# Optimization experiments

Measured on AMD Instinct MI355X. Metric: run time of the kernel, lower is better.

Reference implementation:

```python
import jax, jax.numpy as jnp
from jax import lax
import numpy as np

B, IN, OUT = 32768, 512, 512


def _bit_length(a):
    # a: nonnegative int32. Smear high bit down, then popcount == bit length.
    y = a
    y = y | (y >> 1)
    y = y | (y >> 2)
    y = y | (y >> 4)
    y = y | (y >> 8)
    y = y | (y >> 16)
    return lax.population_count(y)


def trunc_top_bits(v, k=4):
    # compress_top4(|a|,|b|,4): keep top-k significant bits of each magnitude.
    a = jnp.abs(v)
    shift = jnp.maximum(_bit_length(a) - k, 0)
    t = (a >> shift) << shift
    return t * jnp.sign(v)


def setup_inputs() -> dict:
    key = jax.random.key(0)
    k1, k2, k3 = jax.random.split(key, 3)
    bound = 1.0 / np.sqrt(IN)  # matches kaiming_uniform(a=sqrt(5)) + bias bound
    x = jax.random.normal(k1, (B, IN), dtype=jnp.float32)
    weight = jax.random.uniform(k2, (OUT, IN), dtype=jnp.float32, minval=-bound, maxval=bound)
    bias = jax.random.uniform(k3, (OUT,), dtype=jnp.float32, minval=-bound, maxval=bound)
    return {"x": x, "weight": weight, "bias": bias, "weight_sf": 8, "act_sf": 6}


def reference(x, weight, bias, weight_sf, act_sf):
    # Fixed-point quantization: input / 2^{-sf} then trunc-toward-zero int cast
    xi = (x * (2.0 ** act_sf)).astype(jnp.int32)       # [B, IN]
    wi = (weight * (2.0 ** weight_sf)).astype(jnp.int32)  # [OUT, IN]
    # sign/abs decomposition + top-4-bit truncated multiply-accumulate:
    # sum_y compress_top4(|xi|,|wi|) * sign(xi)*sign(wi) == dot of signed truncs
    tx = trunc_top_bits(xi).astype(jnp.float32)
    tw = trunc_top_bits(wi).astype(jnp.float32)
    acc = jnp.einsum("bi,oi->bo", tx, tw)             # [B, OUT], exact in fp32
    scale = (2.0 ** (-act_sf)) * (2.0 ** (-weight_sf))
    return acc * scale + bias[None, :]
```

## Files before the change

kernel.cpp:

```cpp
#include <hip/hip_runtime.h>
#include <hip/hip_bf16.h>
#include <stdint.h>

#define B_DIM 32768
#define IN_DIM 512
#define OUT_DIM 512

typedef __bf16 bf16;
typedef bf16 bf16x8 __attribute__((ext_vector_type(8)));
typedef float f32x4 __attribute__((ext_vector_type(4)));

__device__ __forceinline__ uint32_t quant2(float a, float b, float scale) {
    uint32_t ua = __float_as_uint(truncf(a * scale));
    uint32_t ub = __float_as_uint(truncf(b * scale));
    uint32_t p = __builtin_amdgcn_perm(ub, ua, 0x07060302u);
    return p & 0xFFF0FFF0u;
}

__global__ void quant_kernel(const float* __restrict__ in, bf16* __restrict__ out,
                             int n4, const int* __restrict__ sf) {
    int i = blockIdx.x * blockDim.x + threadIdx.x;
    if (i >= n4) return;
    float scale = (float)(1 << *sf);
    float4 v = ((const float4*)in)[i];
    uint2 p;
    p.x = quant2(v.x, v.y, scale);
    p.y = quant2(v.z, v.w, scale);
    ((uint2*)out)[i] = p;
}

__global__ __launch_bounds__(256, 4)
void gemm_bt(const bf16* __restrict__ A, const bf16* __restrict__ W,
             const float* __restrict__ bias, float* __restrict__ C,
             const int* __restrict__ wsf, const int* __restrict__ asf) {
    __shared__ bf16 As[128 * 64];
    __shared__ bf16 Bs[128 * 64];

    const int t    = threadIdx.x;
    const int w    = t >> 6;
    const int lane = t & 63;

    const int b    = blockIdx.x;
    const int xcd  = b & 7;
    const int slot = b >> 3;
    const int bm   = xcd * 32 + (slot >> 2);
    const int bn   = slot & 3;
    const int row0 = bm * 128;
    const int col0 = bn * 128;
    const int wm   = (w & 1) * 64;
    const int wn   = (w >> 1) * 64;

    const int m_st = t >> 3;
    const int ku   = (t & 7) ^ (m_st & 7);
    const size_t offA = (size_t)(row0 + m_st) * IN_DIM + ku * 8;
    const size_t offB = (size_t)(col0 + m_st) * IN_DIM + ku * 8;

    f32x4 acc[4][4];
    #pragma unroll
    for (int mt = 0; mt < 4; ++mt)
        #pragma unroll
        for (int nt = 0; nt < 4; ++nt)
            acc[mt][nt] = 0.0f;

    for (int k0 = 0; k0 < IN_DIM; k0 += 64) {
        #pragma unroll
        for (int i = 0; i < 4; ++i) {
            const bf16* ga = A + offA + (size_t)i * 32 * IN_DIM + k0;
            bf16*       la = As + (i * 256 + w * 64) * 8;
            __builtin_amdgcn_global_load_lds((const __attribute__((address_space(1))) void*)ga,
                                             (__attribute__((address_space(3))) void*)la, 16, 0, 0);
            const bf16* gb = W + offB + (size_t)i * 32 * IN_DIM + k0;
            bf16*       lb = Bs + (i * 256 + w * 64) * 8;
            __builtin_amdgcn_global_load_lds((const __attribute__((address_space(1))) void*)gb,
                                             (__attribute__((address_space(3))) void*)lb, 16, 0, 0);
        }
        __syncthreads();

        const int q  = lane >> 4;
        const int rl = lane & 15;
        const int sx = rl & 7;
        #pragma unroll
        for (int ks = 0; ks < 2; ++ks) {
            const int c = ks * 4 + q;
            const int cs = (c ^ sx) * 8;
            bf16x8 af[4], bfr[4];
            #pragma unroll
            for (int mt = 0; mt < 4; ++mt)
                af[mt] = *(const bf16x8*)(As + (wm + mt * 16 + rl) * 64 + cs);
            #pragma unroll
            for (int nt = 0; nt < 4; ++nt)
                bfr[nt] = *(const bf16x8*)(Bs + (wn + nt * 16 + rl) * 64 + cs);
            #pragma unroll
            for (int mt = 0; mt < 4; ++mt)
                #pragma unroll
                for (int nt = 0; nt < 4; ++nt)
                    acc[mt][nt] = __builtin_amdgcn_mfma_f32_16x16x32_bf16(af[mt], bfr[nt], acc[mt][nt], 0, 0, 0);
        }
        __syncthreads();
    }

    const float oscale = ldexpf(1.0f, -(*wsf + *asf));
    const int cl = lane & 15;
    const int rg = (lane >> 4) * 4;
    #pragma unroll
    for (int nt = 0; nt < 4; ++nt) {
        const int col = col0 + wn + nt * 16 + cl;
        const float bv = bias[col];
        #pragma unroll
        for (int mt = 0; mt < 4; ++mt) {
            f32x4 a = acc[mt][nt];
            #pragma unroll
            for (int r = 0; r < 4; ++r) {
                const int row = row0 + wm + mt * 16 + rg + r;
                C[(size_t)row * OUT_DIM + col] = a[r] * oscale + bv;
            }
        }
    }
}

extern "C" void kernel_launch(void* const* d_in, const int* in_sizes, int n_in,
                              void* d_out, int out_size, void* d_ws, size_t ws_size,
                              hipStream_t stream) {
    const float* x    = (const float*)d_in[0];
    const float* wgt  = (const float*)d_in[1];
    const float* bias = (const float*)d_in[2];
    const int*   wsf  = (const int*)d_in[3];
    const int*   asf  = (const int*)d_in[4];

    bf16* tx = (bf16*)d_ws;
    bf16* tw = (bf16*)((char*)d_ws + (size_t)B_DIM * IN_DIM * sizeof(bf16));

    const int nx4 = B_DIM * IN_DIM / 4;
    const int nw4 = OUT_DIM * IN_DIM / 4;
    quant_kernel<<<(nx4 + 255) / 256, 256, 0, stream>>>(x, tx, nx4, asf);
    quant_kernel<<<(nw4 + 255) / 256, 256, 0, stream>>>(wgt, tw, nw4, wsf);

    const int grid = (B_DIM / 128) * (OUT_DIM / 128);
    gemm_bt<<<grid, 256, 0, stream>>>(tx, tw, bias, (float*)d_out, wsf, asf);
}
```

Measured before the change: 137.7 us.

## Fuse activation quantization into GEMM with register-prefetched fp32 tiles

Drops the separate quantization pass over the activation matrix. The GEMM now reads fp32 X directly, quantizes it to truncated bf16 in registers and writes the result into the swizzled LDS tile. The next k-tile is prefetched into registers while the current one computes, and the occupancy hint drops from 4 to 3 waves. This removes a full write and re-read of the bf16 intermediate, but each X tile is now read in fp32 by the four column blocks, and the A operand no longer uses asynchronous global-to-LDS loads.

```diff
diff --git a/kernel.cpp b/kernel.cpp
--- a/kernel.cpp
+++ b/kernel.cpp
@@ -29,10 +29,10 @@
     ((uint2*)out)[i] = p;
 }
 
-__global__ __launch_bounds__(256, 4)
-void gemm_bt(const bf16* __restrict__ A, const bf16* __restrict__ W,
-             const float* __restrict__ bias, float* __restrict__ C,
-             const int* __restrict__ wsf, const int* __restrict__ asf) {
+__global__ __launch_bounds__(256, 3)
+void gemm_fused(const float* __restrict__ X, const bf16* __restrict__ W,
+                const float* __restrict__ bias, float* __restrict__ C,
+                const int* __restrict__ wsf, const int* __restrict__ asf) {
     __shared__ bf16 As[128 * 64];
     __shared__ bf16 Bs[128 * 64];
 
@@ -51,9 +51,14 @@
     const int wn   = (w >> 1) * 64;
 
     const int m_st = t >> 3;
-    const int ku   = (t & 7) ^ (m_st & 7);
-    const size_t offA = (size_t)(row0 + m_st) * IN_DIM + ku * 8;
-    const size_t offB = (size_t)(col0 + m_st) * IN_DIM + ku * 8;
+    const int kub  = (t & 7) ^ (m_st & 7);
+    const size_t offB = (size_t)(col0 + m_st) * IN_DIM + kub * 8;
+
+    const int r_a = t >> 1;
+    const int h_a = t & 1;
+    const float* xrow = X + (size_t)(row0 + r_a) * IN_DIM + h_a * 32;
+
+    const float ascale = (float)(1 << *asf);
 
     f32x4 acc[4][4];
     #pragma unroll
@@ -62,26 +67,55 @@
         for (int nt = 0; nt < 4; ++nt)
             acc[mt][nt] = 0.0f;
 
+    float4 fr[8];
+    #pragma unroll
+    for (int j = 0; j < 8; ++j)
+        fr[j] = *((const float4*)xrow + j);
+    uint4 pk[4];
+    #pragma unroll
+    for (int j = 0; j < 4; ++j) {
+        pk[j].x = quant2(fr[2 * j].x, fr[2 * j].y, ascale);
+        pk[j].y = quant2(fr[2 * j].z, fr[2 * j].w, ascale);
+        pk[j].z = quant2(fr[2 * j + 1].x, fr[2 * j + 1].y, ascale);
+        pk[j].w = quant2(fr[2 * j + 1].z, fr[2 * j + 1].w, ascale);
+    }
+
     for (int k0 = 0; k0 < IN_DIM; k0 += 64) {
         #pragma unroll
+        for (int j = 0; j < 4; ++j) {
+            bf16* adst = As + (size_t)(r_a * 8 + ((h_a * 4 + j) ^ (r_a & 7))) * 8;
+            *(uint4*)adst = pk[j];
+        }
+        #pragma unroll
         for (int i = 0; i < 4; ++i) {
-            const bf16* ga = A + offA + (size_t)i * 32 * IN_DIM + k0;
-            bf16*       la = As + (i * 256 + w * 64) * 8;
-            __builtin_amdgcn_global_load_lds((const __attribute__((address_space(1))) void*)ga,
-                                             (__attribute__((address_space(3))) void*)la, 16, 0, 0);
             const bf16* gb = W + offB + (size_t)i * 32 * IN_DIM + k0;
             bf16*       lb = Bs + (i * 256 + w * 64) * 8;
             __builtin_amdgcn_global_load_lds((const __attribute__((address_space(1))) void*)gb,
                                              (__attribute__((address_space(3))) void*)lb, 16, 0, 0);
         }
+        const bool more = (k0 + 64) < IN_DIM;
+        if (more) {
+            #pragma unroll
+            for (int j = 0; j < 8; ++j)
+                fr[j] = *((const float4*)(xrow + k0 + 64) + j);
+        }
         __syncthreads();
+        if (more) {
+            #pragma unroll
+            for (int j = 0; j < 4; ++j) {
+                pk[j].x = quant2(fr[2 * j].x, fr[2 * j].y, ascale);
+                pk[j].y = quant2(fr[2 * j].z, fr[2 * j].w, ascale);
+                pk[j].z = quant2(fr[2 * j + 1].x, fr[2 * j + 1].y, ascale);
+                pk[j].w = quant2(fr[2 * j + 1].z, fr[2 * j + 1].w, ascale);
+            }
+        }
 
         const int q  = lane >> 4;
         const int rl = lane & 15;
         const int sx = rl & 7;
         #pragma unroll
         for (int ks = 0; ks < 2; ++ks) {
-            const int c = ks * 4 + q;
+            const int c  = ks * 4 + q;
             const int cs = (c ^ sx) * 8;
             bf16x8 af[4], bfr[4];
             #pragma unroll
@@ -127,14 +161,11 @@
     const int*   wsf  = (const int*)d_in[3];
     const int*   asf  = (const int*)d_in[4];
 
-    bf16* tx = (bf16*)d_ws;
-    bf16* tw = (bf16*)((char*)d_ws + (size_t)B_DIM * IN_DIM * sizeof(bf16));
+    bf16* tw = (bf16*)d_ws;
 
-    const int nx4 = B_DIM * IN_DIM / 4;
     const int nw4 = OUT_DIM * IN_DIM / 4;
-    quant_kernel<<<(nx4 + 255) / 256, 256, 0, stream>>>(x, tx, nx4, asf);
     quant_kernel<<<(nw4 + 255) / 256, 256, 0, stream>>>(wgt, tw, nw4, wsf);
 
     const int grid = (B_DIM / 128) * (OUT_DIM / 128);
-    gemm_bt<<<grid, 256, 0, stream>>>(tx, tw, bias, (float*)d_out, wsf, asf);
+    gemm_fused<<<grid, 256, 0, stream>>>(x, tw, bias, (float*)d_out, wsf, asf);
 }
```

Result: slower. 155.4 us (+12.8%).

## Quantize operands to FP8 and use FP8 MFMA instead of BF16

Applied to the files above, without the earlier changes.

The quantize kernels now write the top-4-bit truncated values as packed e4m3 FP8 bytes instead of BF16. The GEMM loads byte tiles into LDS with a reworked swizzle and uses the 16x16x32 FP8 MFMA. This halves the bytes written by the quantize pass and read by the GEMM. It relies on every truncated value fitting exactly in e4m3, meaning 3 mantissa bits and a maximum magnitude below 448. It also changes the LDS access pattern, which could introduce bank conflicts.

```diff
diff --git a/kernel.cpp b/kernel.cpp
--- a/kernel.cpp
+++ b/kernel.cpp
@@ -1,40 +1,35 @@
 #include <hip/hip_runtime.h>
-#include <hip/hip_bf16.h>
 #include <stdint.h>
 
 #define B_DIM 32768
 #define IN_DIM 512
 #define OUT_DIM 512
 
-typedef __bf16 bf16;
-typedef bf16 bf16x8 __attribute__((ext_vector_type(8)));
 typedef float f32x4 __attribute__((ext_vector_type(4)));
 
-__device__ __forceinline__ uint32_t quant2(float a, float b, float scale) {
-    uint32_t ua = __float_as_uint(truncf(a * scale));
-    uint32_t ub = __float_as_uint(truncf(b * scale));
-    uint32_t p = __builtin_amdgcn_perm(ub, ua, 0x07060302u);
-    return p & 0xFFF0FFF0u;
+__device__ __forceinline__ float trunc4(float x, float s) {
+    uint32_t u = __float_as_uint(truncf(x * s));
+    return __uint_as_float(u & 0xFFF00000u);
 }
 
-__global__ void quant_kernel(const float* __restrict__ in, bf16* __restrict__ out,
-                             int n4, const int* __restrict__ sf) {
+__global__ void quant_fp8(const float* __restrict__ in, uint32_t* __restrict__ out,
+                          int n4, const int* __restrict__ sf) {
     int i = blockIdx.x * blockDim.x + threadIdx.x;
     if (i >= n4) return;
     float scale = (float)(1 << *sf);
     float4 v = ((const float4*)in)[i];
-    uint2 p;
-    p.x = quant2(v.x, v.y, scale);
-    p.y = quant2(v.z, v.w, scale);
-    ((uint2*)out)[i] = p;
+    int p = 0;
+    p = __builtin_amdgcn_cvt_pk_fp8_f32(trunc4(v.x, scale), trunc4(v.y, scale), p, false);
+    p = __builtin_amdgcn_cvt_pk_fp8_f32(trunc4(v.z, scale), trunc4(v.w, scale), p, true);
+    out[i] = (uint32_t)p;
 }
 
 __global__ __launch_bounds__(256, 4)
-void gemm_bt(const bf16* __restrict__ A, const bf16* __restrict__ W,
+void gemm_f8(const uint8_t* __restrict__ A, const uint8_t* __restrict__ W,
              const float* __restrict__ bias, float* __restrict__ C,
              const int* __restrict__ wsf, const int* __restrict__ asf) {
-    __shared__ bf16 As[128 * 64];
-    __shared__ bf16 Bs[128 * 64];
+    __shared__ uint8_t As[128 * 64];
+    __shared__ uint8_t Bs[128 * 64];
 
     const int t    = threadIdx.x;
     const int w    = t >> 6;
@@ -50,10 +45,10 @@
     const int wm   = (w & 1) * 64;
     const int wn   = (w >> 1) * 64;
 
-    const int m_st = t >> 3;
-    const int ku   = (t & 7) ^ (m_st & 7);
-    const size_t offA = (size_t)(row0 + m_st) * IN_DIM + ku * 8;
-    const size_t offB = (size_t)(col0 + m_st) * IN_DIM + ku * 8;
+    const int m_st = t >> 2;
+    const int goff = ((2 * (t & 3)) ^ (m_st & 6)) * 8;
+    const size_t offA = (size_t)(row0 + m_st) * IN_DIM + goff;
+    const size_t offB = (size_t)(col0 + m_st) * IN_DIM + goff;
 
     f32x4 acc[4][4];
     #pragma unroll
@@ -64,13 +59,13 @@
 
     for (int k0 = 0; k0 < IN_DIM; k0 += 64) {
         #pragma unroll
-        for (int i = 0; i < 4; ++i) {
-            const bf16* ga = A + offA + (size_t)i * 32 * IN_DIM + k0;
-            bf16*       la = As + (i * 256 + w * 64) * 8;
+        for (int i = 0; i < 2; ++i) {
+            const uint8_t* ga = A + offA + (size_t)i * 64 * IN_DIM + k0;
+            uint8_t*       la = As + i * 4096 + w * 1024;
             __builtin_amdgcn_global_load_lds((const __attribute__((address_space(1))) void*)ga,
                                              (__attribute__((address_space(3))) void*)la, 16, 0, 0);
-            const bf16* gb = W + offB + (size_t)i * 32 * IN_DIM + k0;
-            bf16*       lb = Bs + (i * 256 + w * 64) * 8;
+            const uint8_t* gb = W + offB + (size_t)i * 64 * IN_DIM + k0;
+            uint8_t*       lb = Bs + i * 4096 + w * 1024;
             __builtin_amdgcn_global_load_lds((const __attribute__((address_space(1))) void*)gb,
                                              (__attribute__((address_space(3))) void*)lb, 16, 0, 0);
         }
@@ -78,23 +73,23 @@
 
         const int q  = lane >> 4;
         const int rl = lane & 15;
-        const int sx = rl & 7;
+        const int sx = rl & 6;
         #pragma unroll
         for (int ks = 0; ks < 2; ++ks) {
-            const int c = ks * 4 + q;
-            const int cs = (c ^ sx) * 8;
-            bf16x8 af[4], bfr[4];
+            const int c  = ks * 4 + q;
+            const int cb = (c ^ sx) * 8;
+            long af[4], bfr[4];
             #pragma unroll
             for (int mt = 0; mt < 4; ++mt)
-                af[mt] = *(const bf16x8*)(As + (wm + mt * 16 + rl) * 64 + cs);
+                af[mt] = *(const long*)(As + (wm + mt * 16 + rl) * 64 + cb);
             #pragma unroll
             for (int nt = 0; nt < 4; ++nt)
-                bfr[nt] = *(const bf16x8*)(Bs + (wn + nt * 16 + rl) * 64 + cs);
+                bfr[nt] = *(const long*)(Bs + (wn + nt * 16 + rl) * 64 + cb);
             #pragma unroll
             for (int mt = 0; mt < 4; ++mt)
                 #pragma unroll
                 for (int nt = 0; nt < 4; ++nt)
-                    acc[mt][nt] = __builtin_amdgcn_mfma_f32_16x16x32_bf16(af[mt], bfr[nt], acc[mt][nt], 0, 0, 0);
+                    acc[mt][nt] = __builtin_amdgcn_mfma_f32_16x16x32_fp8_fp8(af[mt], bfr[nt], acc[mt][nt], 0, 0, 0);
         }
         __syncthreads();
     }
@@ -127,14 +122,14 @@
     const int*   wsf  = (const int*)d_in[3];
     const int*   asf  = (const int*)d_in[4];
 
-    bf16* tx = (bf16*)d_ws;
-    bf16* tw = (bf16*)((char*)d_ws + (size_t)B_DIM * IN_DIM * sizeof(bf16));
+    uint8_t* tx = (uint8_t*)d_ws;
+    uint8_t* tw = (uint8_t*)d_ws + (size_t)B_DIM * IN_DIM;
 
     const int nx4 = B_DIM * IN_DIM / 4;
     const int nw4 = OUT_DIM * IN_DIM / 4;
-    quant_kernel<<<(nx4 + 255) / 256, 256, 0, stream>>>(x, tx, nx4, asf);
-    quant_kernel<<<(nw4 + 255) / 256, 256, 0, stream>>>(wgt, tw, nw4, wsf);
+    quant_fp8<<<(nx4 + 255) / 256, 256, 0, stream>>>(x, (uint32_t*)tx, nx4, asf);
+    quant_fp8<<<(nw4 + 255) / 256, 256, 0, stream>>>(wgt, (uint32_t*)tw, nw4, wsf);
 
     const int grid = (B_DIM / 128) * (OUT_DIM / 128);
-    gemm_bt<<<grid, 256, 0, stream>>>(tx, tw, bias, (float*)d_out, wsf, asf);
+    gemm_f8<<<grid, 256, 0, stream>>>(tx, tw, bias, (float*)d_out, wsf, asf);
 }
```

Result: no change. 135.1 us (-1.9%).
